# Optimization experiments

Measured on AMD Instinct MI355X. Metric: run time of the kernel, lower is better.

Reference implementation:

```python
import jax, jax.numpy as jnp
import numpy as np

B = 16
NUM_CN = 25000
NUM_VN = 50000
NUM_EDGES = 200000
D_EMBED = 16
D_HIDDEN = 32
D_MSG = 16


def setup_inputs() -> dict:
    key = jax.random.key(0)
    ks = jax.random.split(key, 16)
    def w(k, fan_in, fan_out):
        return jax.random.normal(k, (fan_in, fan_out), dtype=jnp.float32) / jnp.sqrt(jnp.float32(fan_in))
    return {
        "h_from_x": jax.random.normal(ks[0], (B, NUM_CN, D_EMBED), dtype=jnp.float32),
        "h_from_z": jax.random.normal(ks[1], (B, NUM_CN, D_EMBED), dtype=jnp.float32),
        "h_to": jax.random.normal(ks[2], (B, NUM_VN, D_EMBED), dtype=jnp.float32),
        "syndrome_x": jax.random.randint(ks[3], (B, NUM_CN), 0, 2, dtype=jnp.int32),
        "syndrome_z": jax.random.randint(ks[4], (B, NUM_CN), 0, 2, dtype=jnp.int32),
        "from_ind_x": jax.random.randint(ks[5], (NUM_EDGES,), 0, NUM_CN, dtype=jnp.int32),
        "to_ind_x": jax.random.randint(ks[6], (NUM_EDGES,), 0, NUM_VN, dtype=jnp.int32),
        "from_ind_z": jax.random.randint(ks[7], (NUM_EDGES,), 0, NUM_CN, dtype=jnp.int32),
        "to_ind_z": jax.random.randint(ks[8], (NUM_EDGES,), 0, NUM_VN, dtype=jnp.int32),
        # msg MLP x: [2*D_EMBED -> D_HIDDEN (relu) -> D_MSG], no bias
        "Wx1": w(ks[9], 2 * D_EMBED, D_HIDDEN),
        "Wx2": w(ks[10], D_HIDDEN, D_MSG),
        "Wz1": w(ks[11], 2 * D_EMBED, D_HIDDEN),
        "Wz2": w(ks[12], D_HIDDEN, D_MSG),
        # embed MLP: [2*D_MSG + D_EMBED -> D_HIDDEN (relu) -> D_EMBED], no bias
        "We1": w(ks[13], 2 * D_MSG + D_EMBED, D_HIDDEN),
        "We2": w(ks[14], D_HIDDEN, D_EMBED),
    }


def _edge_messages(h_from, h_to, syn, from_ind, to_ind, W1, W2):
    # gather edge endpoint embeddings -> [B, E, 2*D_EMBED]
    feat = jnp.concatenate([h_from[:, from_ind, :], h_to[:, to_ind, :]], axis=-1)
    msg = jnp.maximum(feat @ W1, 0.0) @ W2          # [B, E, D_MSG]
    mask = syn[:, from_ind].astype(msg.dtype)[..., None]
    return msg * mask


def _segment_reduce_sum(msg, to_ind, num_vn):
    # ragged gather+sum per receiving vertex == segment_sum over to_ind
    # msg: [B, E, D] -> [E, B, D] -> segment_sum -> [N, B, D] -> [B, N, D]
    m = jax.ops.segment_sum(jnp.transpose(msg, (1, 0, 2)), to_ind, num_segments=num_vn)
    return jnp.transpose(m, (1, 0, 2))


def reference(h_from_x, h_from_z, h_to, syndrome_x, syndrome_z,
              from_ind_x, to_ind_x, from_ind_z, to_ind_z,
              Wx1, Wx2, Wz1, Wz2, We1, We2):
    num_vn = h_to.shape[1]
    msg_x = _edge_messages(h_from_x, h_to, syndrome_x, from_ind_x, to_ind_x, Wx1, Wx2)
    msg_z = _edge_messages(h_from_z, h_to, syndrome_z, from_ind_z, to_ind_z, Wz1, Wz2)
    m_x = _segment_reduce_sum(msg_x, to_ind_x, num_vn)  # [B, N, D_MSG]
    m_z = _segment_reduce_sum(msg_z, to_ind_z, num_vn)
    feat = jnp.concatenate([m_x, m_z, h_to], axis=-1)   # [B, N, 2*D_MSG+D_EMBED]
    h_to_new = jnp.maximum(feat @ We1, 0.0) @ We2
    return h_to_new
```

## Files before the change

kernel.cpp:

```cpp
#include <hip/hip_runtime.h>

#define NUM_CN   25000
#define NUM_VN   50000
#define NUM_E    200000
#define D_EMBED  16
#define D_HIDDEN 32
#define D_MSG    16
#define BATCH    16

#define WS_IDS_X   0
#define WS_IDS_Z   200000
#define WS_OFF_X   400000
#define WS_OFF_Z   450001
#define WS_CNT_X   500002
#define WS_CNT_Z   550002
#define WS_CUR_X   600002
#define WS_CUR_Z   650002
#define WS_INCL_X  700002
#define WS_INCL_Z  751202
#define WS_PSUM    802402
#define WS_BASE    802530
#define WS_A1X     802816
#define WS_A1Z     7202816
#define SCAN_CHUNKS 49

__global__ __launch_bounds__(256) void hist_kernel(
    const int* __restrict__ ti_x, const int* __restrict__ ti_z,
    int* __restrict__ cnt_x, int* __restrict__ cnt_z)
{
    int e = blockIdx.x * 256 + threadIdx.x;
    if (e >= NUM_E) return;
    atomicAdd(&cnt_x[ti_x[e]], 1);
    atomicAdd(&cnt_z[ti_z[e]], 1);
}

__global__ __launch_bounds__(1024) void scan1_kernel(
    const int* __restrict__ cnt_x, const int* __restrict__ cnt_z,
    int* __restrict__ incl_x, int* __restrict__ incl_z,
    int* __restrict__ psum)
{
    __shared__ int s[1024];
    const int ch  = blockIdx.y;
    const int blk = blockIdx.x;
    const int t   = threadIdx.x;
    const int gid = blk * 1024 + t;
    const int* cnt  = ch ? cnt_z  : cnt_x;
    int*       incl = ch ? incl_z : incl_x;
    int v = (gid < NUM_VN) ? cnt[gid] : 0;
    s[t] = v;
    __syncthreads();
#pragma unroll
    for (int d = 1; d < 1024; d <<= 1) {
        int x = 0;
        if (t >= d) x = s[t - d];
        __syncthreads();
        if (t >= d) s[t] += x;
        __syncthreads();
    }
    incl[gid] = s[t];
    if (t == 1023) psum[ch * 64 + blk] = s[1023];
}

__global__ void scan2_kernel(const int* __restrict__ psum, int* __restrict__ base)
{
    int ch = threadIdx.x;
    if (ch >= 2) return;
    int run = 0;
    for (int i = 0; i < SCAN_CHUNKS; ++i) {
        base[ch * 64 + i] = run;
        run += psum[ch * 64 + i];
    }
}

__global__ __launch_bounds__(1024) void scan3_kernel(
    const int* __restrict__ cnt_x, const int* __restrict__ cnt_z,
    const int* __restrict__ incl_x, const int* __restrict__ incl_z,
    const int* __restrict__ base,
    int* __restrict__ off_x, int* __restrict__ off_z,
    int* __restrict__ cur_x, int* __restrict__ cur_z)
{
    const int ch  = blockIdx.y;
    const int blk = blockIdx.x;
    const int t   = threadIdx.x;
    const int i   = blk * 1024 + t;
    if (i >= NUM_VN) return;
    const int* cnt  = ch ? cnt_z  : cnt_x;
    const int* incl = ch ? incl_z : incl_x;
    int*       off  = ch ? off_z  : off_x;
    int*       cur  = ch ? cur_z  : cur_x;
    int bs = base[ch * 64 + blk];
    int iv = incl[i];
    off[i + 1] = bs + iv;
    cur[i]     = bs + iv - cnt[i];
    if (i == 0) off[0] = 0;
}

__global__ __launch_bounds__(256) void fill_kernel(
    const int* __restrict__ ti_x, const int* __restrict__ ti_z,
    const int* __restrict__ fi_x, const int* __restrict__ fi_z,
    int* __restrict__ cur_x, int* __restrict__ cur_z,
    int* __restrict__ ids_x, int* __restrict__ ids_z)
{
    int e = blockIdx.x * 256 + threadIdx.x;
    if (e >= NUM_E) return;
    int px = atomicAdd(&cur_x[ti_x[e]], 1);
    ids_x[px] = fi_x[e];
    int pz = atomicAdd(&cur_z[ti_z[e]], 1);
    ids_z[pz] = fi_z[e];
}

__global__ __launch_bounds__(256) void pack_bits_kernel(
    const int* __restrict__ syn_x, const int* __restrict__ syn_z,
    unsigned* __restrict__ bits_x, unsigned* __restrict__ bits_z)
{
    int cn = blockIdx.x * 256 + threadIdx.x;
    if (cn >= NUM_CN) return;
    unsigned wx = 0, wz = 0;
#pragma unroll
    for (int b = 0; b < BATCH; ++b) {
        wx |= (unsigned)(syn_x[b * NUM_CN + cn] & 1) << b;
        wz |= (unsigned)(syn_z[b * NUM_CN + cn] & 1) << b;
    }
    bits_x[cn] = wx;
    bits_z[cn] = wz;
}

__device__ __forceinline__ unsigned pack_bf16(float a, float b) {
    unsigned ua = __float_as_uint(a); ua += 0x7fff + ((ua >> 16) & 1);
    unsigned ub = __float_as_uint(b); ub += 0x7fff + ((ub >> 16) & 1);
    return (ua >> 16) | (ub & 0xffff0000u);
}

__global__ __launch_bounds__(256) void a1_kernel(
    const float* __restrict__ h_from_x, const float* __restrict__ h_from_z,
    const float* __restrict__ Wx1, const float* __restrict__ Wz1,
    uint4* __restrict__ a1x, uint4* __restrict__ a1z)
{
    int t = blockIdx.x * 256 + threadIdx.x;
    if (t >= NUM_CN * BATCH) return;
    const int ch = blockIdx.y;
    const int b  = t & 15;
    const int cn = t >> 4;
    const float* hsrc = (ch ? h_from_z : h_from_x) + ((size_t)b * NUM_CN + cn) * D_EMBED;
    const float* W1   = ch ? Wz1 : Wx1;
    uint4* dst = (ch ? a1z : a1x) + (size_t)cn * 64;

    float hf[D_EMBED];
#pragma unroll
    for (int i = 0; i < 4; ++i) {
        float4 v = ((const float4*)hsrc)[i];
        hf[4 * i + 0] = v.x; hf[4 * i + 1] = v.y;
        hf[4 * i + 2] = v.z; hf[4 * i + 3] = v.w;
    }
    float a[D_HIDDEN];
#pragma unroll
    for (int j = 0; j < D_HIDDEN; ++j) a[j] = 0.0f;
#pragma unroll
    for (int i = 0; i < D_EMBED; ++i) {
        const float fi = hf[i];
#pragma unroll
        for (int j = 0; j < D_HIDDEN; ++j)
            a[j] = fmaf(fi, W1[i * D_HIDDEN + j], a[j]);
    }
    unsigned u[16];
#pragma unroll
    for (int j = 0; j < 16; ++j) u[j] = pack_bf16(a[2 * j], a[2 * j + 1]);
#pragma unroll
    for (int p = 0; p < 4; ++p) {
        uint4 q;
        q.x = u[4 * p + 0]; q.y = u[4 * p + 1];
        q.z = u[4 * p + 2]; q.w = u[4 * p + 3];
        dst[p * 16 + b] = q;
    }
}

__device__ __forceinline__ void channel_accum(
    const float* __restrict__ h_to_slot, int n, int b,
    const int* __restrict__ off, const int* __restrict__ ids,
    const unsigned* __restrict__ bits,
    const uint4* __restrict__ a1,
    const float* __restrict__ W1, const float* __restrict__ W2,
    unsigned* __restrict__ um)
{
    float ht[D_EMBED];
#pragma unroll
    for (int i = 0; i < 4; ++i) {
        float4 v = ((const float4*)h_to_slot)[i];
        ht[4 * i + 0] = v.x; ht[4 * i + 1] = v.y;
        ht[4 * i + 2] = v.z; ht[4 * i + 3] = v.w;
    }
    float2 a2[16];
#pragma unroll
    for (int p = 0; p < 16; ++p) { a2[p].x = 0.0f; a2[p].y = 0.0f; }
#pragma unroll
    for (int i = 0; i < D_EMBED; ++i) {
        const float hi = ht[i];
        const float* w = W1 + (D_EMBED + i) * D_HIDDEN;
#pragma unroll
        for (int p = 0; p < 16; ++p) {
            a2[p].x = fmaf(hi, w[2 * p],     a2[p].x);
            a2[p].y = fmaf(hi, w[2 * p + 1], a2[p].y);
        }
    }

    float2 hacc[16];
#pragma unroll
    for (int p = 0; p < 16; ++p) { hacc[p].x = 0.0f; hacc[p].y = 0.0f; }

    const int ks = off[n], ke = off[n + 1];
    for (int k = ks; k < ke; ++k) {
        const int from = ids[k];
        const unsigned mw = bits[from];
        const uint4* pa = a1 + (size_t)from * 64 + b;
        uint4 q0 = pa[0], q1 = pa[16], q2 = pa[32], q3 = pa[48];
        const float fm = (float)((mw >> b) & 1u);
        unsigned uu[16] = {q0.x, q0.y, q0.z, q0.w,
                           q1.x, q1.y, q1.z, q1.w,
                           q2.x, q2.y, q2.z, q2.w,
                           q3.x, q3.y, q3.z, q3.w};
#pragma unroll
        for (int p = 0; p < 16; ++p) {
            float lo = __uint_as_float(uu[p] << 16);
            float hi = __uint_as_float(uu[p] & 0xffff0000u);
            hacc[p].x = fmaf(fm, fmaxf(a2[p].x + lo, 0.0f), hacc[p].x);
            hacc[p].y = fmaf(fm, fmaxf(a2[p].y + hi, 0.0f), hacc[p].y);
        }
    }

    float m[D_MSG];
#pragma unroll
    for (int j = 0; j < D_MSG; ++j) m[j] = 0.0f;
#pragma unroll
    for (int p = 0; p < 16; ++p) {
        const float h0 = hacc[p].x, h1 = hacc[p].y;
        const float* w0 = W2 + (2 * p) * D_MSG;
        const float* w1 = W2 + (2 * p + 1) * D_MSG;
#pragma unroll
        for (int j = 0; j < D_MSG; ++j)
            m[j] = fmaf(h0, w0[j], fmaf(h1, w1[j], m[j]));
    }
#pragma unroll
    for (int j = 0; j < 8; ++j) um[j] = pack_bf16(m[2 * j], m[2 * j + 1]);
}

__global__ __launch_bounds__(256) void gather_kernel(
    const float* __restrict__ h_to,
    const unsigned* __restrict__ bits_x, const unsigned* __restrict__ bits_z,
    const int* __restrict__ off_x, const int* __restrict__ ids_x,
    const int* __restrict__ off_z, const int* __restrict__ ids_z,
    const uint4* __restrict__ a1x, const uint4* __restrict__ a1z,
    const float* __restrict__ Wx1, const float* __restrict__ Wx2,
    const float* __restrict__ Wz1, const float* __restrict__ Wz2,
    uint4* __restrict__ out_m)
{
    const int t = blockIdx.x * 256 + threadIdx.x;
    if (t >= NUM_VN * BATCH) return;
    const int b = t & (BATCH - 1);
    const int n = t >> 4;
    const size_t slot = (size_t)b * NUM_VN + n;
    const float* ht_slot = h_to + slot * D_EMBED;

    unsigned um[16];
    channel_accum(ht_slot, n, b, off_x, ids_x, bits_x, a1x, Wx1, Wx2, um);
    channel_accum(ht_slot, n, b, off_z, ids_z, bits_z, a1z, Wz1, Wz2, um + 8);

    uint4* dst = out_m + slot * 4;
#pragma unroll
    for (int p = 0; p < 4; ++p) {
        uint4 q;
        q.x = um[4 * p + 0]; q.y = um[4 * p + 1];
        q.z = um[4 * p + 2]; q.w = um[4 * p + 3];
        dst[p] = q;
    }
}

__global__ __launch_bounds__(256) void node_kernel(
    const float* __restrict__ h_to,
    const float* __restrict__ We1, const float* __restrict__ We2,
    float* out)
{
    const int t = blockIdx.x * 256 + threadIdx.x;
    if (t >= NUM_VN * BATCH) return;
    const int b = t & (BATCH - 1);
    const int n = t >> 4;
    const size_t slot = (size_t)b * NUM_VN + n;

    const uint4* pm = (const uint4*)out + slot * 4;
    uint4 q0 = pm[0], q1 = pm[1], q2 = pm[2], q3 = pm[3];
    unsigned uu[16] = {q0.x, q0.y, q0.z, q0.w,
                       q1.x, q1.y, q1.z, q1.w,
                       q2.x, q2.y, q2.z, q2.w,
                       q3.x, q3.y, q3.z, q3.w};
    float f[48];
#pragma unroll
    for (int p = 0; p < 16; ++p) {
        f[2 * p]     = __uint_as_float(uu[p] << 16);
        f[2 * p + 1] = __uint_as_float(uu[p] & 0xffff0000u);
    }
#pragma unroll
    for (int i = 0; i < 4; ++i) {
        float4 v = ((const float4*)(h_to + slot * D_EMBED))[i];
        f[32 + 4 * i + 0] = v.x; f[32 + 4 * i + 1] = v.y;
        f[32 + 4 * i + 2] = v.z; f[32 + 4 * i + 3] = v.w;
    }

    float2 hid[16];
#pragma unroll
    for (int p = 0; p < 16; ++p) { hid[p].x = 0.0f; hid[p].y = 0.0f; }
#pragma unroll
    for (int i = 0; i < 48; ++i) {
        const float fi = f[i];
        const float* w = We1 + i * D_HIDDEN;
#pragma unroll
        for (int p = 0; p < 16; ++p) {
            hid[p].x = fmaf(fi, w[2 * p],     hid[p].x);
            hid[p].y = fmaf(fi, w[2 * p + 1], hid[p].y);
        }
    }
#pragma unroll
    for (int p = 0; p < 16; ++p) {
        hid[p].x = fmaxf(hid[p].x, 0.0f);
        hid[p].y = fmaxf(hid[p].y, 0.0f);
    }

    float o[D_EMBED];
#pragma unroll
    for (int k = 0; k < D_EMBED; ++k) o[k] = 0.0f;
#pragma unroll
    for (int p = 0; p < 16; ++p) {
        const float h0 = hid[p].x, h1 = hid[p].y;
        const float* w0 = We2 + (2 * p) * D_EMBED;
        const float* w1 = We2 + (2 * p + 1) * D_EMBED;
#pragma unroll
        for (int k = 0; k < D_EMBED; ++k)
            o[k] = fmaf(h0, w0[k], fmaf(h1, w1[k], o[k]));
    }

#pragma unroll
    for (int i = 0; i < 4; ++i) {
        float4 v;
        v.x = o[4 * i + 0]; v.y = o[4 * i + 1];
        v.z = o[4 * i + 2]; v.w = o[4 * i + 3];
        ((float4*)(out + slot * D_EMBED))[i] = v;
    }
}

extern "C" void kernel_launch(void* const* d_in, const int* in_sizes, int n_in,
                              void* d_out, int out_size, void* d_ws, size_t ws_size,
                              hipStream_t stream) {
    const float* h_from_x = (const float*)d_in[0];
    const float* h_from_z = (const float*)d_in[1];
    const float* h_to     = (const float*)d_in[2];
    const int*   syn_x    = (const int*)d_in[3];
    const int*   syn_z    = (const int*)d_in[4];
    const int*   fi_x     = (const int*)d_in[5];
    const int*   ti_x     = (const int*)d_in[6];
    const int*   fi_z     = (const int*)d_in[7];
    const int*   ti_z     = (const int*)d_in[8];
    const float* Wx1      = (const float*)d_in[9];
    const float* Wx2      = (const float*)d_in[10];
    const float* Wz1      = (const float*)d_in[11];
    const float* Wz2      = (const float*)d_in[12];
    const float* We1      = (const float*)d_in[13];
    const float* We2      = (const float*)d_in[14];

    int* ws = (int*)d_ws;
    int* ids_x  = ws + WS_IDS_X;
    int* ids_z  = ws + WS_IDS_Z;
    int* off_x  = ws + WS_OFF_X;
    int* off_z  = ws + WS_OFF_Z;
    int* cnt_x  = ws + WS_CNT_X;
    int* cnt_z  = ws + WS_CNT_Z;
    int* cur_x  = ws + WS_CUR_X;
    int* cur_z  = ws + WS_CUR_Z;
    int* incl_x = ws + WS_INCL_X;
    int* incl_z = ws + WS_INCL_Z;
    int* psum   = ws + WS_PSUM;
    int* base   = ws + WS_BASE;
    uint4* a1x  = (uint4*)(ws + WS_A1X);
    uint4* a1z  = (uint4*)(ws + WS_A1Z);

    unsigned* bits_x = (unsigned*)cur_x;
    unsigned* bits_z = (unsigned*)cur_z;

    hipMemsetAsync(cnt_x, 0, 2 * NUM_VN * sizeof(int), stream);

    hist_kernel<<<dim3((NUM_E + 255) / 256), dim3(256), 0, stream>>>(
        ti_x, ti_z, cnt_x, cnt_z);
    scan1_kernel<<<dim3(SCAN_CHUNKS, 2), dim3(1024), 0, stream>>>(
        cnt_x, cnt_z, incl_x, incl_z, psum);
    scan2_kernel<<<dim3(1), dim3(64), 0, stream>>>(psum, base);
    scan3_kernel<<<dim3(SCAN_CHUNKS, 2), dim3(1024), 0, stream>>>(
        cnt_x, cnt_z, incl_x, incl_z, base, off_x, off_z, cur_x, cur_z);
    fill_kernel<<<dim3((NUM_E + 255) / 256), dim3(256), 0, stream>>>(
        ti_x, ti_z, fi_x, fi_z, cur_x, cur_z, ids_x, ids_z);
    pack_bits_kernel<<<dim3((NUM_CN + 255) / 256), dim3(256), 0, stream>>>(
        syn_x, syn_z, bits_x, bits_z);

    a1_kernel<<<dim3((NUM_CN * BATCH + 255) / 256, 2), dim3(256), 0, stream>>>(
        h_from_x, h_from_z, Wx1, Wz1, a1x, a1z);

    gather_kernel<<<dim3((NUM_VN * BATCH) / 256), dim3(256), 0, stream>>>(
        h_to, bits_x, bits_z, off_x, ids_x, off_z, ids_z, a1x, a1z,
        Wx1, Wx2, Wz1, Wz2, (uint4*)d_out);

    node_kernel<<<dim3((NUM_VN * BATCH) / 256), dim3(256), 0, stream>>>(
        h_to, We1, We2, (float*)d_out);
}
```

Measured before the change: 419.4 us.

## Fuse preprocessing kernels, fold syndrome mask into A1, unroll gather loop

Merges the histogram and syndrome bit-pack into one launch and replaces the three-kernel scan with a single two-block scan kernel, cutting launch count. The syndrome mask moves into a1_kernel: masked entries are written as bf16 -inf, so ReLU(a2 + a1) gives zero and the gather loop no longer loads mask bits per edge. The gather edge loop is unrolled by two so two edges' loads are in flight at once. The single-block scan serializes 49 elements per thread, and the -inf trick relies on a2 staying finite.

Result: slower. 559.2 us (+33.3%).

```diff
diff --git a/kernel.cpp b/kernel.cpp
--- a/kernel.cpp
+++ b/kernel.cpp
@@ -16,83 +16,78 @@
 #define WS_CNT_Z   550002
 #define WS_CUR_X   600002
 #define WS_CUR_Z   650002
-#define WS_INCL_X  700002
-#define WS_INCL_Z  751202
-#define WS_PSUM    802402
-#define WS_BASE    802530
+#define WS_BITS_X  700002
+#define WS_BITS_Z  725002
 #define WS_A1X     802816
 #define WS_A1Z     7202816
-#define SCAN_CHUNKS 49
-
-__global__ __launch_bounds__(256) void hist_kernel(
+
+#define E_BLOCKS   782
+#define CN_BLOCKS  98
+
+__global__ __launch_bounds__(256) void histpack_kernel(
     const int* __restrict__ ti_x, const int* __restrict__ ti_z,
-    int* __restrict__ cnt_x, int* __restrict__ cnt_z)
-{
-    int e = blockIdx.x * 256 + threadIdx.x;
-    if (e >= NUM_E) return;
-    atomicAdd(&cnt_x[ti_x[e]], 1);
-    atomicAdd(&cnt_z[ti_z[e]], 1);
-}
-
-__global__ __launch_bounds__(1024) void scan1_kernel(
+    int* __restrict__ cnt_x, int* __restrict__ cnt_z,
+    const int* __restrict__ syn_x, const int* __restrict__ syn_z,
+    unsigned* __restrict__ bits_x, unsigned* __restrict__ bits_z)
+{
+    if (blockIdx.x < E_BLOCKS) {
+        int e = blockIdx.x * 256 + threadIdx.x;
+        if (e >= NUM_E) return;
+        atomicAdd(&cnt_x[ti_x[e]], 1);
+        atomicAdd(&cnt_z[ti_z[e]], 1);
+    } else {
+        int cn = (blockIdx.x - E_BLOCKS) * 256 + threadIdx.x;
+        if (cn >= NUM_CN) return;
+        unsigned wx = 0, wz = 0;
+#pragma unroll
+        for (int b = 0; b < BATCH; ++b) {
+            wx |= (unsigned)(syn_x[b * NUM_CN + cn] & 1) << b;
+            wz |= (unsigned)(syn_z[b * NUM_CN + cn] & 1) << b;
+        }
+        bits_x[cn] = wx;
+        bits_z[cn] = wz;
+    }
+}
+
+__global__ __launch_bounds__(1024) void scan_kernel(
     const int* __restrict__ cnt_x, const int* __restrict__ cnt_z,
-    int* __restrict__ incl_x, int* __restrict__ incl_z,
-    int* __restrict__ psum)
-{
-    __shared__ int s[1024];
-    const int ch  = blockIdx.y;
-    const int blk = blockIdx.x;
-    const int t   = threadIdx.x;
-    const int gid = blk * 1024 + t;
-    const int* cnt  = ch ? cnt_z  : cnt_x;
-    int*       incl = ch ? incl_z : incl_x;
-    int v = (gid < NUM_VN) ? cnt[gid] : 0;
-    s[t] = v;
+    int* __restrict__ off_x, int* __restrict__ off_z,
+    int* __restrict__ cur_x, int* __restrict__ cur_z)
+{
+    __shared__ int sh[1024];
+    const int ch = blockIdx.x;
+    const int t  = threadIdx.x;
+    const int* cnt = ch ? cnt_z : cnt_x;
+    int*       off = ch ? off_z : off_x;
+    int*       cur = ch ? cur_z : cur_x;
+
+    const int base_i = t * 49;
+    int s = 0;
+    for (int i = 0; i < 49; ++i) {
+        int idx = base_i + i;
+        if (idx < NUM_VN) s += cnt[idx];
+    }
+    sh[t] = s;
     __syncthreads();
 #pragma unroll
     for (int d = 1; d < 1024; d <<= 1) {
         int x = 0;
-        if (t >= d) x = s[t - d];
+        if (t >= d) x = sh[t - d];
         __syncthreads();
-        if (t >= d) s[t] += x;
+        if (t >= d) sh[t] += x;
         __syncthreads();
     }
-    incl[gid] = s[t];
-    if (t == 1023) psum[ch * 64 + blk] = s[1023];
-}
-
-__global__ void scan2_kernel(const int* __restrict__ psum, int* __restrict__ base)
-{
-    int ch = threadIdx.x;
-    if (ch >= 2) return;
-    int run = 0;
-    for (int i = 0; i < SCAN_CHUNKS; ++i) {
-        base[ch * 64 + i] = run;
-        run += psum[ch * 64 + i];
-    }
-}
-
-__global__ __launch_bounds__(1024) void scan3_kernel(
-    const int* __restrict__ cnt_x, const int* __restrict__ cnt_z,
-    const int* __restrict__ incl_x, const int* __restrict__ incl_z,
-    const int* __restrict__ base,
-    int* __restrict__ off_x, int* __restrict__ off_z,
-    int* __restrict__ cur_x, int* __restrict__ cur_z)
-{
-    const int ch  = blockIdx.y;
-    const int blk = blockIdx.x;
-    const int t   = threadIdx.x;
-    const int i   = blk * 1024 + t;
-    if (i >= NUM_VN) return;
-    const int* cnt  = ch ? cnt_z  : cnt_x;
-    const int* incl = ch ? incl_z : incl_x;
-    int*       off  = ch ? off_z  : off_x;
-    int*       cur  = ch ? cur_z  : cur_x;
-    int bs = base[ch * 64 + blk];
-    int iv = incl[i];
-    off[i + 1] = bs + iv;
-    cur[i]     = bs + iv - cnt[i];
-    if (i == 0) off[0] = 0;
+    int run = sh[t] - s;
+    for (int i = 0; i < 49; ++i) {
+        int idx = base_i + i;
+        if (idx < NUM_VN) {
+            int c = cnt[idx];
+            cur[idx] = run;
+            run += c;
+            off[idx + 1] = run;
+        }
+    }
+    if (t == 0) off[0] = 0;
 }
 
 __global__ __launch_bounds__(256) void fill_kernel(
@@ -109,22 +104,6 @@
     ids_z[pz] = fi_z[e];
 }
 
-__global__ __launch_bounds__(256) void pack_bits_kernel(
-    const int* __restrict__ syn_x, const int* __restrict__ syn_z,
-    unsigned* __restrict__ bits_x, unsigned* __restrict__ bits_z)
-{
-    int cn = blockIdx.x * 256 + threadIdx.x;
-    if (cn >= NUM_CN) return;
-    unsigned wx = 0, wz = 0;
-#pragma unroll
-    for (int b = 0; b < BATCH; ++b) {
-        wx |= (unsigned)(syn_x[b * NUM_CN + cn] & 1) << b;
-        wz |= (unsigned)(syn_z[b * NUM_CN + cn] & 1) << b;
-    }
-    bits_x[cn] = wx;
-    bits_z[cn] = wz;
-}
-
 __device__ __forceinline__ unsigned pack_bf16(float a, float b) {
     unsigned ua = __float_as_uint(a); ua += 0x7fff + ((ua >> 16) & 1);
     unsigned ub = __float_as_uint(b); ub += 0x7fff + ((ub >> 16) & 1);
@@ -134,6 +113,7 @@
 __global__ __launch_bounds__(256) void a1_kernel(
     const float* __restrict__ h_from_x, const float* __restrict__ h_from_z,
     const float* __restrict__ Wx1, const float* __restrict__ Wz1,
+    const unsigned* __restrict__ bits_x, const unsigned* __restrict__ bits_z,
     uint4* __restrict__ a1x, uint4* __restrict__ a1z)
 {
     int t = blockIdx.x * 256 + threadIdx.x;
@@ -143,6 +123,8 @@
     const int cn = t >> 4;
     const float* hsrc = (ch ? h_from_z : h_from_x) + ((size_t)b * NUM_CN + cn) * D_EMBED;
     const float* W1   = ch ? Wz1 : Wx1;
+    const unsigned bw = (ch ? bits_z : bits_x)[cn];
+    const bool on = ((bw >> b) & 1u) != 0u;
     uint4* dst = (ch ? a1z : a1x) + (size_t)cn * 64;
 
     float hf[D_EMBED];
@@ -164,7 +146,10 @@
     }
     unsigned u[16];
 #pragma unroll
-    for (int j = 0; j < 16; ++j) u[j] = pack_bf16(a[2 * j], a[2 * j + 1]);
+    for (int j = 0; j < 16; ++j) {
+        unsigned w = pack_bf16(a[2 * j], a[2 * j + 1]);
+        u[j] = on ? w : 0xFF80FF80u;
+    }
 #pragma unroll
     for (int p = 0; p < 4; ++p) {
         uint4 q;
@@ -174,10 +159,26 @@
     }
 }
 
+__device__ __forceinline__ void acc_edge(
+    float2 hacc[16], const float2 a2[16],
+    uint4 q0, uint4 q1, uint4 q2, uint4 q3)
+{
+    unsigned uu[16] = {q0.x, q0.y, q0.z, q0.w,
+                       q1.x, q1.y, q1.z, q1.w,
+                       q2.x, q2.y, q2.z, q2.w,
+                       q3.x, q3.y, q3.z, q3.w};
+#pragma unroll
+    for (int p = 0; p < 16; ++p) {
+        float lo = __uint_as_float(uu[p] << 16);
+        float hi = __uint_as_float(uu[p] & 0xffff0000u);
+        hacc[p].x += fmaxf(a2[p].x + lo, 0.0f);
+        hacc[p].y += fmaxf(a2[p].y + hi, 0.0f);
+    }
+}
+
 __device__ __forceinline__ void channel_accum(
     const float* __restrict__ h_to_slot, int n, int b,
     const int* __restrict__ off, const int* __restrict__ ids,
-    const unsigned* __restrict__ bits,
     const uint4* __restrict__ a1,
     const float* __restrict__ W1, const float* __restrict__ W2,
     unsigned* __restrict__ um)
@@ -208,23 +209,21 @@
     for (int p = 0; p < 16; ++p) { hacc[p].x = 0.0f; hacc[p].y = 0.0f; }
 
     const int ks = off[n], ke = off[n + 1];
-    for (int k = ks; k < ke; ++k) {
-        const int from = ids[k];
-        const unsigned mw = bits[from];
-        const uint4* pa = a1 + (size_t)from * 64 + b;
-        uint4 q0 = pa[0], q1 = pa[16], q2 = pa[32], q3 = pa[48];
-        const float fm = (float)((mw >> b) & 1u);
-        unsigned uu[16] = {q0.x, q0.y, q0.z, q0.w,
-                           q1.x, q1.y, q1.z, q1.w,
-                           q2.x, q2.y, q2.z, q2.w,
-                           q3.x, q3.y, q3.z, q3.w};
-#pragma unroll
-        for (int p = 0; p < 16; ++p) {
-            float lo = __uint_as_float(uu[p] << 16);
-            float hi = __uint_as_float(uu[p] & 0xffff0000u);
-            hacc[p].x = fmaf(fm, fmaxf(a2[p].x + lo, 0.0f), hacc[p].x);
-            hacc[p].y = fmaf(fm, fmaxf(a2[p].y + hi, 0.0f), hacc[p].y);
-        }
+    int k = ks;
+    for (; k + 2 <= ke; k += 2) {
+        const int f0 = ids[k];
+        const int f1 = ids[k + 1];
+        const uint4* p0 = a1 + (size_t)f0 * 64 + b;
+        const uint4* p1 = a1 + (size_t)f1 * 64 + b;
+        uint4 q0 = p0[0], q1 = p0[16], q2 = p0[32], q3 = p0[48];
+        uint4 r0 = p1[0], r1 = p1[16], r2 = p1[32], r3 = p1[48];
+        acc_edge(hacc, a2, q0, q1, q2, q3);
+        acc_edge(hacc, a2, r0, r1, r2, r3);
+    }
+    if (k < ke) {
+        const int f0 = ids[k];
+        const uint4* p0 = a1 + (size_t)f0 * 64 + b;
+        acc_edge(hacc, a2, p0[0], p0[16], p0[32], p0[48]);
     }
 
     float m[D_MSG];
@@ -245,7 +244,6 @@
 
 __global__ __launch_bounds__(256) void gather_kernel(
     const float* __restrict__ h_to,
-    const unsigned* __restrict__ bits_x, const unsigned* __restrict__ bits_z,
     const int* __restrict__ off_x, const int* __restrict__ ids_x,
     const int* __restrict__ off_z, const int* __restrict__ ids_z,
     const uint4* __restrict__ a1x, const uint4* __restrict__ a1z,
@@ -254,15 +252,14 @@
     uint4* __restrict__ out_m)
 {
     const int t = blockIdx.x * 256 + threadIdx.x;
-    if (t >= NUM_VN * BATCH) return;
     const int b = t & (BATCH - 1);
     const int n = t >> 4;
     const size_t slot = (size_t)b * NUM_VN + n;
     const float* ht_slot = h_to + slot * D_EMBED;
 
     unsigned um[16];
-    channel_accum(ht_slot, n, b, off_x, ids_x, bits_x, a1x, Wx1, Wx2, um);
-    channel_accum(ht_slot, n, b, off_z, ids_z, bits_z, a1z, Wz1, Wz2, um + 8);
+    channel_accum(ht_slot, n, b, off_x, ids_x, a1x, Wx1, Wx2, um);
+    channel_accum(ht_slot, n, b, off_z, ids_z, a1z, Wz1, Wz2, um + 8);
 
     uint4* dst = out_m + slot * 4;
 #pragma unroll
@@ -280,7 +277,6 @@
     float* out)
 {
     const int t = blockIdx.x * 256 + threadIdx.x;
-    if (t >= NUM_VN * BATCH) return;
     const int b = t & (BATCH - 1);
     const int n = t >> 4;
     const size_t slot = (size_t)b * NUM_VN + n;
@@ -365,43 +361,32 @@
     const float* We2      = (const float*)d_in[14];
 
     int* ws = (int*)d_ws;
-    int* ids_x  = ws + WS_IDS_X;
-    int* ids_z  = ws + WS_IDS_Z;
-    int* off_x  = ws + WS_OFF_X;
-    int* off_z  = ws + WS_OFF_Z;
-    int* cnt_x  = ws + WS_CNT_X;
-    int* cnt_z  = ws + WS_CNT_Z;
-    int* cur_x  = ws + WS_CUR_X;
-    int* cur_z  = ws + WS_CUR_Z;
-    int* incl_x = ws + WS_INCL_X;
-    int* incl_z = ws + WS_INCL_Z;
-    int* psum   = ws + WS_PSUM;
-    int* base   = ws + WS_BASE;
-    uint4* a1x  = (uint4*)(ws + WS_A1X);
-    uint4* a1z  = (uint4*)(ws + WS_A1Z);
-
-    unsigned* bits_x = (unsigned*)cur_x;
-    unsigned* bits_z = (unsigned*)cur_z;
+    int*      ids_x  = ws + WS_IDS_X;
+    int*      ids_z  = ws + WS_IDS_Z;
+    int*      off_x  = ws + WS_OFF_X;
+    int*      off_z  = ws + WS_OFF_Z;
+    int*      cnt_x  = ws + WS_CNT_X;
+    int*      cnt_z  = ws + WS_CNT_Z;
+    int*      cur_x  = ws + WS_CUR_X;
+    int*      cur_z  = ws + WS_CUR_Z;
+    unsigned* bits_x = (unsigned*)(ws + WS_BITS_X);
+    unsigned* bits_z = (unsigned*)(ws + WS_BITS_Z);
+    uint4*    a1x    = (uint4*)(ws + WS_A1X);
+    uint4*    a1z    = (uint4*)(ws + WS_A1Z);
 
     hipMemsetAsync(cnt_x, 0, 2 * NUM_VN * sizeof(int), stream);
 
-    hist_kernel<<<dim3((NUM_E + 255) / 256), dim3(256), 0, stream>>>(
-        ti_x, ti_z, cnt_x, cnt_z);
-    scan1_kernel<<<dim3(SCAN_CHUNKS, 2), dim3(1024), 0, stream>>>(
-        cnt_x, cnt_z, incl_x, incl_z, psum);
-    scan2_kernel<<<dim3(1), dim3(64), 0, stream>>>(psum, base);
-    scan3_kernel<<<dim3(SCAN_CHUNKS, 2), dim3(1024), 0, stream>>>(
-        cnt_x, cnt_z, incl_x, incl_z, base, off_x, off_z, cur_x, cur_z);
-    fill_kernel<<<dim3((NUM_E + 255) / 256), dim3(256), 0, stream>>>(
+    histpack_kernel<<<dim3(E_BLOCKS + CN_BLOCKS), dim3(256), 0, stream>>>(
+        ti_x, ti_z, cnt_x, cnt_z, syn_x, syn_z, bits_x, bits_z);
+    scan_kernel<<<dim3(2), dim3(1024), 0, stream>>>(
+        cnt_x, cnt_z, off_x, off_z, cur_x, cur_z);
+    fill_kernel<<<dim3(E_BLOCKS), dim3(256), 0, stream>>>(
         ti_x, ti_z, fi_x, fi_z, cur_x, cur_z, ids_x, ids_z);
-    pack_bits_kernel<<<dim3((NUM_CN + 255) / 256), dim3(256), 0, stream>>>(
-        syn_x, syn_z, bits_x, bits_z);
-
     a1_kernel<<<dim3((NUM_CN * BATCH + 255) / 256, 2), dim3(256), 0, stream>>>(
-        h_from_x, h_from_z, Wx1, Wz1, a1x, a1z);
+        h_from_x, h_from_z, Wx1, Wz1, bits_x, bits_z, a1x, a1z);
 
     gather_kernel<<<dim3((NUM_VN * BATCH) / 256), dim3(256), 0, stream>>>(
-        h_to, bits_x, bits_z, off_x, ids_x, off_z, ids_z, a1x, a1z,
+        h_to, off_x, ids_x, off_z, ids_z, a1x, a1z,
         Wx1, Wx2, Wz1, Wz2, (uint4*)d_out);
 
     node_kernel<<<dim3((NUM_VN * BATCH) / 256), dim3(256), 0, stream>>>(
```
